# Kernel tuning notes

Hardware: AMD Instinct MI355X
Metric: run time of the kernel (lower is better)

The kernel has to match this reference:

```python
import jax, jax.numpy as jnp
import numpy as np

D = 256
H = 8
FFN = 2048
EPS = 1e-5


def _layer_norm(x, g, b):
    m = jnp.mean(x, axis=-1, keepdims=True)
    v = jnp.mean((x - m) ** 2, axis=-1, keepdims=True)
    return (x - m) * jax.lax.rsqrt(v + EPS) * g + b


def _mha(q_in, k_in, v_in, wq, bq, wk, bk, wv, bv, wo, bo, mask):
    B, Sq, _ = q_in.shape
    Sk = k_in.shape[1]
    dh = D // H
    q = (q_in @ wq + bq).reshape(B, Sq, H, dh)
    k = (k_in @ wk + bk).reshape(B, Sk, H, dh)
    v = (v_in @ wv + bv).reshape(B, Sk, H, dh)
    scores = jnp.einsum('bqhd,bkhd->bhqk', q, k) / jnp.sqrt(jnp.float32(dh)).astype(q.dtype)
    if mask is not None:
        scores = scores + mask
    probs = jax.nn.softmax(scores, axis=-1)
    ctx = jnp.einsum('bhqk,bkhd->bqhd', probs, v).reshape(B, Sq, D)
    return ctx @ wo + bo


def setup_inputs() -> dict:
    key = jax.random.key(0)
    ks = jax.random.split(key, 32)
    s = 0.02
    def lin(i, din, dout):
        return jax.random.normal(ks[i], (din, dout), jnp.float32) * s
    inp = {
        'vision_encoder_hidden_states': jax.random.normal(ks[0], (4, 2048, D), jnp.float32),
        'text_encoder_hidden_states': jax.random.normal(ks[1], (4, 1024, D), jnp.float32),
        'vision_encoder_attention_mask': jnp.zeros((4, 1, 1, 2048), jnp.float32),
        'text_encoder_attention_mask': jnp.zeros((4, 1, 1, 1024), jnp.float32),
        'sa_wq': lin(2, D, D), 'sa_bq': jnp.zeros((D,), jnp.float32),
        'sa_wk': lin(3, D, D), 'sa_bk': jnp.zeros((D,), jnp.float32),
        'sa_wv': lin(4, D, D), 'sa_bv': jnp.zeros((D,), jnp.float32),
        'sa_wo': lin(5, D, D), 'sa_bo': jnp.zeros((D,), jnp.float32),
        'ca_wq': lin(6, D, D), 'ca_bq': jnp.zeros((D,), jnp.float32),
        'ca_wk': lin(7, D, D), 'ca_bk': jnp.zeros((D,), jnp.float32),
        'ca_wv': lin(8, D, D), 'ca_bv': jnp.zeros((D,), jnp.float32),
        'ca_wo': lin(9, D, D), 'ca_bo': jnp.zeros((D,), jnp.float32),
        'ln1_g': jnp.ones((D,), jnp.float32), 'ln1_b': jnp.zeros((D,), jnp.float32),
        'ln2_g': jnp.ones((D,), jnp.float32), 'ln2_b': jnp.zeros((D,), jnp.float32),
        'ln3_g': jnp.ones((D,), jnp.float32), 'ln3_b': jnp.zeros((D,), jnp.float32),
        'ln4_g': jnp.ones((D,), jnp.float32), 'ln4_b': jnp.zeros((D,), jnp.float32),
        'fc1_w': lin(10, D, FFN), 'fc1_b': jnp.zeros((FFN,), jnp.float32),
        'fc2_w': lin(11, FFN, D), 'fc2_b': jnp.zeros((D,), jnp.float32),
    }
    return inp


def reference(vision_encoder_hidden_states, text_encoder_hidden_states,
              vision_encoder_attention_mask, text_encoder_attention_mask,
              sa_wq, sa_bq, sa_wk, sa_bk, sa_wv, sa_bv, sa_wo, sa_bo,
              ca_wq, ca_bq, ca_wk, ca_bk, ca_wv, ca_bv, ca_wo, ca_bo,
              ln1_g, ln1_b, ln2_g, ln2_b, ln3_g, ln3_b, ln4_g, ln4_b,
              fc1_w, fc1_b, fc2_w, fc2_b):
    # self-attention over vision queries (dropout = identity in eval)
    residual = vision_encoder_hidden_states
    h = _mha(vision_encoder_hidden_states, vision_encoder_hidden_states,
             vision_encoder_hidden_states,
             sa_wq, sa_bq, sa_wk, sa_bk, sa_wv, sa_bv, sa_wo, sa_bo,
             vision_encoder_attention_mask)
    h = _layer_norm(residual + h, ln1_g, ln1_b)
    # text cross-attention
    res2 = h
    h = _mha(h, text_encoder_hidden_states, text_encoder_hidden_states,
             ca_wq, ca_bq, ca_wk, ca_bk, ca_wv, ca_bv, ca_wo, ca_bo,
             text_encoder_attention_mask)
    h = _layer_norm(res2 + h, ln2_g, ln2_b)
    # third block: residual + dropout(h) -> in eval this is h + h = 2h, then LN
    h = _layer_norm(h + h, ln3_g, ln3_b)
    # FFN
    res = h
    h = jax.nn.relu(h @ fc1_w + fc1_b)
    h = h @ fc2_w + fc2_b
    h = _layer_norm(res + h, ln4_g, ln4_b)
    return h
```

## Files before the change

### kernel.cpp

```cpp
#include <hip/hip_runtime.h>
#include <stdint.h>
#include <stddef.h>

#define HEADS 8
#define DH 32
#define DMODEL 256
#define LN_EPS 1e-5f
#define LOG2E 1.4426950408889634f
#define QSCALE 0.17677669529663687f
#define QSCALE2 (QSCALE * LOG2E)
#define EXP2(x) __builtin_amdgcn_exp2f(x)

typedef unsigned short u16;
typedef __bf16 bf16x8 __attribute__((ext_vector_type(8)));
typedef unsigned short u16x8 __attribute__((ext_vector_type(8)));
typedef float f32x4 __attribute__((ext_vector_type(4)));

static __device__ __forceinline__ u16 bfc(float f) {
    return __builtin_bit_cast(u16, (__bf16)f);
}
static __device__ __forceinline__ bf16x8 ldbf8(const u16* p) {
    return __builtin_bit_cast(bf16x8, *reinterpret_cast<const u16x8*>(p));
}
static __device__ __forceinline__ bf16x8 cvt8(float4 a, float4 b) {
    bf16x8 r;
    r[0] = (__bf16)a.x; r[1] = (__bf16)a.y; r[2] = (__bf16)a.z; r[3] = (__bf16)a.w;
    r[4] = (__bf16)b.x; r[5] = (__bf16)b.y; r[6] = (__bf16)b.z; r[7] = (__bf16)b.w;
    return r;
}

struct TDesc { const float* src; u16* dst; int K; int N; };
struct TArgs { TDesc d[10]; };

__global__ __launch_bounds__(256) void transpose_cvt(TArgs args) {
    TDesc d = args.d[blockIdx.y];
    const int ntx = d.N >> 5;
    const int tiles = (d.K >> 5) * ntx;
    if ((int)blockIdx.x >= tiles) return;
    const int tk = (blockIdx.x / ntx) << 5;
    const int tn = (blockIdx.x % ntx) << 5;
    __shared__ float t[32][33];
    const int lx = threadIdx.x & 31;
    const int ly = threadIdx.x >> 5;
#pragma unroll
    for (int i = 0; i < 4; ++i)
        t[ly + 8 * i][lx] = d.src[(size_t)(tk + ly + 8 * i) * d.N + tn + lx];
    __syncthreads();
#pragma unroll
    for (int i = 0; i < 4; ++i)
        d.dst[(size_t)(tn + ly + 8 * i) * d.K + tk + lx] = bfc(t[lx][ly + 8 * i]);
}

struct Slice { u16* out; const float* bias; int mode; float sc; };

__global__ __launch_bounds__(256) void gemm_xproj(
    const float* __restrict__ Af, const u16* __restrict__ Wt,
    Slice s0, Slice s1, Slice s2, int M, int ntm)
{
    const int lane = threadIdx.x & 63;
    const int wave = threadIdx.x >> 6;
    const int l15 = lane & 15, lhi = lane >> 4;
    const int tm = ((int)blockIdx.x % ntm) * 128;
    const int tn = ((int)blockIdx.x / ntm) * 64;
    const int wm = tm + wave * 32;
    const int sel = tn >> 8;
    const int tl = tn & 255;
    Slice sl = (sel == 0) ? s0 : (sel == 1 ? s1 : s2);

    const f32x4 z4 = {0.f, 0.f, 0.f, 0.f};
    f32x4 acc[2][4];
#pragma unroll
    for (int i = 0; i < 2; ++i)
#pragma unroll
        for (int j = 0; j < 4; ++j) acc[i][j] = z4;

    const float* ar0 = Af + (size_t)(wm + l15) * 256 + lhi * 8;
    const float* ar1 = ar0 + (size_t)16 * 256;
    const u16* b0p = Wt + (size_t)(tn + l15) * 256 + lhi * 8;

    float4 a00 = *(const float4*)(ar0), a01 = *(const float4*)(ar0 + 4);
    float4 a10 = *(const float4*)(ar1), a11 = *(const float4*)(ar1 + 4);
    bf16x8 b[4];
#pragma unroll
    for (int j = 0; j < 4; ++j) b[j] = ldbf8(b0p + (size_t)j * 16 * 256);

#pragma unroll
    for (int k = 32; k < 256; k += 32) {
        float4 n00 = *(const float4*)(ar0 + k), n01 = *(const float4*)(ar0 + k + 4);
        float4 n10 = *(const float4*)(ar1 + k), n11 = *(const float4*)(ar1 + k + 4);
        bf16x8 bn[4];
#pragma unroll
        for (int j = 0; j < 4; ++j) bn[j] = ldbf8(b0p + (size_t)j * 16 * 256 + k);
        bf16x8 a0 = cvt8(a00, a01), a1 = cvt8(a10, a11);
#pragma unroll
        for (int j = 0; j < 4; ++j) {
            acc[0][j] = __builtin_amdgcn_mfma_f32_16x16x32_bf16(a0, b[j], acc[0][j], 0, 0, 0);
            acc[1][j] = __builtin_amdgcn_mfma_f32_16x16x32_bf16(a1, b[j], acc[1][j], 0, 0, 0);
        }
        a00 = n00; a01 = n01; a10 = n10; a11 = n11;
#pragma unroll
        for (int j = 0; j < 4; ++j) b[j] = bn[j];
    }
    {
        bf16x8 a0 = cvt8(a00, a01), a1 = cvt8(a10, a11);
#pragma unroll
        for (int j = 0; j < 4; ++j) {
            acc[0][j] = __builtin_amdgcn_mfma_f32_16x16x32_bf16(a0, b[j], acc[0][j], 0, 0, 0);
            acc[1][j] = __builtin_amdgcn_mfma_f32_16x16x32_bf16(a1, b[j], acc[1][j], 0, 0, 0);
        }
    }

#pragma unroll
    for (int i = 0; i < 2; ++i) {
#pragma unroll
        for (int j = 0; j < 4; ++j) {
            const int col = tl + j * 16 + l15;
            const float bv = sl.bias[col];
            const int row0 = wm + i * 16 + lhi * 4;
            if (sl.mode == 1) {
#pragma unroll
                for (int r = 0; r < 4; ++r)
                    sl.out[(size_t)(row0 + r) * 256 + col] = bfc((acc[i][j][r] + bv) * sl.sc);
            } else {
                ushort4 o = make_ushort4(bfc((acc[i][j][0] + bv) * sl.sc), bfc((acc[i][j][1] + bv) * sl.sc),
                                         bfc((acc[i][j][2] + bv) * sl.sc), bfc((acc[i][j][3] + bv) * sl.sc));
                *reinterpret_cast<ushort4*>(sl.out + (size_t)col * M + row0) = o;
            }
        }
    }
}

template<int MODE, bool RELU>
__global__ __launch_bounds__(256) void gemm_wide(
    const u16* __restrict__ A, const u16* __restrict__ Bt,
    const float* __restrict__ bias, void* __restrict__ Cout,
    int M, int N, int K, int ntm, float osc)
{
    const int lane = threadIdx.x & 63;
    const int wave = threadIdx.x >> 6;
    const int l15 = lane & 15, lhi = lane >> 4;
    const int tm = ((int)blockIdx.x % ntm) * 128;
    const int tn = ((int)blockIdx.x / ntm) * 128;
    const int wm = tm + wave * 32;

    const f32x4 z4 = {0.f, 0.f, 0.f, 0.f};
    f32x4 acc[2][8];
#pragma unroll
    for (int i = 0; i < 2; ++i)
#pragma unroll
        for (int j = 0; j < 8; ++j) acc[i][j] = z4;

    const u16* a0p = A + (size_t)(wm + l15) * K + lhi * 8;
    const u16* a1p = a0p + (size_t)16 * K;
    const u16* b0p = Bt + (size_t)(tn + l15) * K + lhi * 8;

    bf16x8 a0 = ldbf8(a0p), a1 = ldbf8(a1p);
    bf16x8 b[8];
#pragma unroll
    for (int j = 0; j < 8; ++j) b[j] = ldbf8(b0p + (size_t)j * 16 * K);

    for (int k = 32; k < K; k += 32) {
        bf16x8 a0n = ldbf8(a0p + k), a1n = ldbf8(a1p + k);
        bf16x8 bn[8];
#pragma unroll
        for (int j = 0; j < 8; ++j) bn[j] = ldbf8(b0p + (size_t)j * 16 * K + k);
#pragma unroll
        for (int j = 0; j < 8; ++j) {
            acc[0][j] = __builtin_amdgcn_mfma_f32_16x16x32_bf16(a0, b[j], acc[0][j], 0, 0, 0);
            acc[1][j] = __builtin_amdgcn_mfma_f32_16x16x32_bf16(a1, b[j], acc[1][j], 0, 0, 0);
        }
        a0 = a0n; a1 = a1n;
#pragma unroll
        for (int j = 0; j < 8; ++j) b[j] = bn[j];
    }
#pragma unroll
    for (int j = 0; j < 8; ++j) {
        acc[0][j] = __builtin_amdgcn_mfma_f32_16x16x32_bf16(a0, b[j], acc[0][j], 0, 0, 0);
        acc[1][j] = __builtin_amdgcn_mfma_f32_16x16x32_bf16(a1, b[j], acc[1][j], 0, 0, 0);
    }

#pragma unroll
    for (int i = 0; i < 2; ++i) {
#pragma unroll
        for (int j = 0; j < 8; ++j) {
            const int col = tn + j * 16 + l15;
            const float bv = bias[col];
            const int row0 = wm + i * 16 + lhi * 4;
            if (MODE == 0) {
                float* C = (float*)Cout;
#pragma unroll
                for (int r = 0; r < 4; ++r) {
                    float v = acc[i][j][r] + bv;
                    if (RELU) v = fmaxf(v, 0.f);
                    C[(size_t)(row0 + r) * N + col] = v;
                }
            } else {
                u16* C = (u16*)Cout;
#pragma unroll
                for (int r = 0; r < 4; ++r) {
                    float v = acc[i][j][r] + bv;
                    if (RELU) v = fmaxf(v, 0.f);
                    C[(size_t)(row0 + r) * N + col] = bfc(v * osc);
                }
            }
        }
    }
}

__global__ __launch_bounds__(256) void gemm_sk2(
    const u16* __restrict__ A, const u16* __restrict__ Bt,
    const float* __restrict__ bias, float* __restrict__ Cout,
    int M, int N, int lda, int Kh, int ntm)
{
    const int kh = (int)blockIdx.x >= (ntm * (N / 64));
    const int bid = (int)blockIdx.x - kh * (ntm * (N / 64));
    const int lane = threadIdx.x & 63;
    const int wave = threadIdx.x >> 6;
    const int l15 = lane & 15, lhi = lane >> 4;
    const int tm = (bid % ntm) * 128;
    const int tn = (bid / ntm) * 64;
    const int wm = tm + wave * 32;

    const f32x4 z4 = {0.f, 0.f, 0.f, 0.f};
    f32x4 acc[2][4];
#pragma unroll
    for (int i = 0; i < 2; ++i)
#pragma unroll
        for (int j = 0; j < 4; ++j) acc[i][j] = z4;

    const u16* a0p = A + (size_t)(wm + l15) * lda + kh * Kh + lhi * 8;
    const u16* a1p = a0p + (size_t)16 * lda;
    const u16* b0p = Bt + (size_t)(tn + l15) * lda + kh * Kh + lhi * 8;

    bf16x8 a0 = ldbf8(a0p), a1 = ldbf8(a1p);
    bf16x8 b[4];
#pragma unroll
    for (int j = 0; j < 4; ++j) b[j] = ldbf8(b0p + (size_t)j * 16 * lda);

    for (int k = 32; k < Kh; k += 32) {
        bf16x8 a0n = ldbf8(a0p + k), a1n = ldbf8(a1p + k);
        bf16x8 bn[4];
#pragma unroll
        for (int j = 0; j < 4; ++j) bn[j] = ldbf8(b0p + (size_t)j * 16 * lda + k);
#pragma unroll
        for (int j = 0; j < 4; ++j) {
            acc[0][j] = __builtin_amdgcn_mfma_f32_16x16x32_bf16(a0, b[j], acc[0][j], 0, 0, 0);
            acc[1][j] = __builtin_amdgcn_mfma_f32_16x16x32_bf16(a1, b[j], acc[1][j], 0, 0, 0);
        }
        a0 = a0n; a1 = a1n;
#pragma unroll
        for (int j = 0; j < 4; ++j) b[j] = bn[j];
    }
#pragma unroll
    for (int j = 0; j < 4; ++j) {
        acc[0][j] = __builtin_amdgcn_mfma_f32_16x16x32_bf16(a0, b[j], acc[0][j], 0, 0, 0);
        acc[1][j] = __builtin_amdgcn_mfma_f32_16x16x32_bf16(a1, b[j], acc[1][j], 0, 0, 0);
    }

    float* C = Cout + (size_t)kh * M * N;
    const float bs = kh ? 0.f : 1.f;
#pragma unroll
    for (int i = 0; i < 2; ++i) {
#pragma unroll
        for (int j = 0; j < 4; ++j) {
            const int col = tn + j * 16 + l15;
            const float bv = bias[col] * bs;
            const int row0 = wm + i * 16 + lhi * 4;
#pragma unroll
            for (int r = 0; r < 4; ++r)
                C[(size_t)(row0 + r) * N + col] = acc[i][j][r] + bv;
        }
    }
}

template<int MODE, bool RELU>
__global__ __launch_bounds__(256) void gemm64(
    const u16* __restrict__ A, const u16* __restrict__ Bt,
    const float* __restrict__ bias, void* __restrict__ Cout,
    int M, int N, int K, int ntn, float osc)
{
    const int lane = threadIdx.x & 63;
    const int wave = threadIdx.x >> 6;
    const int l15 = lane & 15, lhi = lane >> 4;
    const int tn = ((int)blockIdx.x % ntn) * 64;
    const int tm = ((int)blockIdx.x / ntn) * 64;
    const int wm = tm + (wave & 1) * 32;
    const int wn = tn + (wave >> 1) * 32;

    const f32x4 z4 = {0.f, 0.f, 0.f, 0.f};
    f32x4 acc[2][2] = {{z4, z4}, {z4, z4}};

    const u16* a0p = A + (size_t)(wm + l15) * K + lhi * 8;
    const u16* a1p = a0p + (size_t)16 * K;
    const u16* b0p = Bt + (size_t)(wn + l15) * K + lhi * 8;
    const u16* b1p = b0p + (size_t)16 * K;

    bf16x8 aA0 = ldbf8(a0p), aA1 = ldbf8(a1p), bA0 = ldbf8(b0p), bA1 = ldbf8(b1p);
    bf16x8 aB0 = ldbf8(a0p + 32), aB1 = ldbf8(a1p + 32), bB0 = ldbf8(b0p + 32), bB1 = ldbf8(b1p + 32);

#define G64_MFMA(aX0, aX1, bX0, bX1)                                                        \
    acc[0][0] = __builtin_amdgcn_mfma_f32_16x16x32_bf16(aX0, bX0, acc[0][0], 0, 0, 0);      \
    acc[0][1] = __builtin_amdgcn_mfma_f32_16x16x32_bf16(aX0, bX1, acc[0][1], 0, 0, 0);      \
    acc[1][0] = __builtin_amdgcn_mfma_f32_16x16x32_bf16(aX1, bX0, acc[1][0], 0, 0, 0);      \
    acc[1][1] = __builtin_amdgcn_mfma_f32_16x16x32_bf16(aX1, bX1, acc[1][1], 0, 0, 0);

    for (int k = 64; k < K; k += 64) {
        G64_MFMA(aA0, aA1, bA0, bA1);
        aA0 = ldbf8(a0p + k); aA1 = ldbf8(a1p + k);
        bA0 = ldbf8(b0p + k); bA1 = ldbf8(b1p + k);
        G64_MFMA(aB0, aB1, bB0, bB1);
        aB0 = ldbf8(a0p + k + 32); aB1 = ldbf8(a1p + k + 32);
        bB0 = ldbf8(b0p + k + 32); bB1 = ldbf8(b1p + k + 32);
    }
    G64_MFMA(aA0, aA1, bA0, bA1);
    G64_MFMA(aB0, aB1, bB0, bB1);
#undef G64_MFMA

#pragma unroll
    for (int i = 0; i < 2; ++i) {
#pragma unroll
        for (int j = 0; j < 2; ++j) {
            const int col = wn + j * 16 + l15;
            const float bv = bias[col];
            const int row0 = wm + i * 16 + lhi * 4;
            if (MODE == 0) {
                float* C = (float*)Cout;
#pragma unroll
                for (int r = 0; r < 4; ++r) {
                    float v = acc[i][j][r] + bv;
                    if (RELU) v = fmaxf(v, 0.f);
                    C[(size_t)(row0 + r) * N + col] = v;
                }
            } else {
                u16* C = (u16*)Cout;
#pragma unroll
                for (int r = 0; r < 4; ++r) {
                    float v = acc[i][j][r] + bv;
                    if (RELU) v = fmaxf(v, 0.f);
                    C[(size_t)(row0 + r) * N + col] = bfc(v * osc);
                }
            }
        }
    }
}

__global__ __launch_bounds__(256) void attn_kernel(
    const u16* __restrict__ Qb, const u16* __restrict__ Kb,
    const u16* __restrict__ Vt, const float* __restrict__ mask,
    u16* __restrict__ Ob, int Sq, int Sk, int MkTot)
{
    const int wave = threadIdx.x >> 6;
    const int lane = threadIdx.x & 63;
    const int l15 = lane & 15, lhi = lane >> 4;
    const int nqc = Sq >> 7;

    const int nwg = (int)gridDim.x;
    const int p = (int)blockIdx.x;
    const int wgid = (p & 7) * (nwg >> 3) + (p >> 3);

    const int bh = wgid / nqc;
    const int qc = wgid % nqc;
    const int b = bh >> 3;
    const int h = bh & 7;
    const int colh = h * DH;
    const int qrow0 = b * Sq + (qc << 7) + wave * 32;
    const int swz = (l15 & 8) << 1;

    __shared__ __align__(16) u16 pt[4][32][72];

    const f32x4 z4 = {0.f, 0.f, 0.f, 0.f};
    const bf16x8 qf0 = ldbf8(Qb + (size_t)(qrow0 + l15) * DMODEL + colh + lhi * 8);
    const bf16x8 qf1 = ldbf8(Qb + (size_t)(qrow0 + 16 + l15) * DMODEL + colh + lhi * 8);

    f32x4 ctx[2][2] = {{z4, z4}, {z4, z4}};
    float m0 = -1e30f, m1 = -1e30f, ss0 = 0.f, ss1 = 0.f;

    const float* mb = mask + (size_t)b * Sk;
    const u16* kbase = Kb + (size_t)(b * Sk) * DMODEL + colh + lhi * 8;
    const u16* vbase = Vt + (size_t)colh * MkTot + (size_t)b * Sk;

    bf16x8 kf[4], vf[4];
    float4 mk[4];
#pragma unroll
    for (int j = 0; j < 4; ++j)
        kf[j] = ldbf8(kbase + (size_t)(j * 16 + l15) * DMODEL);
#pragma unroll
    for (int ks = 0; ks < 2; ++ks)
#pragma unroll
        for (int dt = 0; dt < 2; ++dt)
            vf[ks * 2 + dt] = ldbf8(vbase + (size_t)(dt * 16 + l15) * MkTot + ks * 32 + lhi * 8);
#pragma unroll
    for (int j = 0; j < 4; ++j) {
        float4 t0 = *reinterpret_cast<const float4*>(mb + j * 16 + lhi * 4);
        mk[j] = make_float4(t0.x * LOG2E, t0.y * LOG2E, t0.z * LOG2E, t0.w * LOG2E);
    }

    for (int kt = 0; kt < Sk; kt += 64) {
        f32x4 s[2][4];
#pragma unroll
        for (int j = 0; j < 4; ++j) {
            s[0][j] = __builtin_amdgcn_mfma_f32_16x16x32_bf16(kf[j], qf0, z4, 0, 0, 0);
            s[1][j] = __builtin_amdgcn_mfma_f32_16x16x32_bf16(kf[j], qf1, z4, 0, 0, 0);
        }

        const int ktn = (kt + 64 < Sk) ? kt + 64 : kt;
        bf16x8 kn[4], vn[4];
        float4 mn[4];
#pragma unroll
        for (int j = 0; j < 4; ++j)
            kn[j] = ldbf8(kbase + (size_t)(ktn + j * 16 + l15) * DMODEL);
#pragma unroll
        for (int ks = 0; ks < 2; ++ks)
#pragma unroll
            for (int dt = 0; dt < 2; ++dt)
                vn[ks * 2 + dt] = ldbf8(vbase + (size_t)(dt * 16 + l15) * MkTot + ktn + ks * 32 + lhi * 8);
#pragma unroll
        for (int j = 0; j < 4; ++j)
            mn[j] = *reinterpret_cast<const float4*>(mb + ktn + j * 16 + lhi * 4);

#pragma unroll
        for (int j = 0; j < 4; ++j) {
            s[0][j][0] += mk[j].x; s[1][j][0] += mk[j].x;
            s[0][j][1] += mk[j].y; s[1][j][1] += mk[j].y;
            s[0][j][2] += mk[j].z; s[1][j][2] += mk[j].z;
            s[0][j][3] += mk[j].w; s[1][j][3] += mk[j].w;
        }

        float mx0 = fmaxf(fmaxf(s[0][0][0], s[0][0][1]), fmaxf(s[0][0][2], s[0][0][3]));
        float mx1 = fmaxf(fmaxf(s[1][0][0], s[1][0][1]), fmaxf(s[1][0][2], s[1][0][3]));
#pragma unroll
        for (int j = 1; j < 4; ++j) {
            mx0 = fmaxf(mx0, fmaxf(fmaxf(s[0][j][0], s[0][j][1]), fmaxf(s[0][j][2], s[0][j][3])));
            mx1 = fmaxf(mx1, fmaxf(fmaxf(s[1][j][0], s[1][j][1]), fmaxf(s[1][j][2], s[1][j][3])));
        }

        if (!__all((mx0 - m0 <= 12.0f) && (mx1 - m1 <= 12.0f))) {
            mx0 = fmaxf(mx0, __shfl_xor(mx0, 16, 64));
            mx0 = fmaxf(mx0, __shfl_xor(mx0, 32, 64));
            mx1 = fmaxf(mx1, __shfl_xor(mx1, 16, 64));
            mx1 = fmaxf(mx1, __shfl_xor(mx1, 32, 64));
            float n0 = fmaxf(m0, mx0), n1 = fmaxf(m1, mx1);
            float c0 = EXP2(m0 - n0), c1 = EXP2(m1 - n1);
            m0 = n0; m1 = n1; ss0 *= c0; ss1 *= c1;
#pragma unroll
            for (int r = 0; r < 4; ++r) {
                float cc0 = __shfl(c0, lhi * 4 + r, 64);
                float cc1 = __shfl(c1, lhi * 4 + r, 64);
                ctx[0][0][r] *= cc0; ctx[0][1][r] *= cc0;
                ctx[1][0][r] *= cc1; ctx[1][1][r] *= cc1;
            }
        }

        float pa0 = 0.f, pb0 = 0.f, pc0 = 0.f, pd0 = 0.f;
        float pa1 = 0.f, pb1 = 0.f, pc1 = 0.f, pd1 = 0.f;
#pragma unroll
        for (int j = 0; j < 4; ++j) {
            float e00 = EXP2(s[0][j][0] - m0), e01 = EXP2(s[0][j][1] - m0);
            float e02 = EXP2(s[0][j][2] - m0), e03 = EXP2(s[0][j][3] - m0);
            float e10 = EXP2(s[1][j][0] - m1), e11 = EXP2(s[1][j][1] - m1);
            float e12 = EXP2(s[1][j][2] - m1), e13 = EXP2(s[1][j][3] - m1);
            s[0][j][0] = e00; s[0][j][1] = e01; s[0][j][2] = e02; s[0][j][3] = e03;
            s[1][j][0] = e10; s[1][j][1] = e11; s[1][j][2] = e12; s[1][j][3] = e13;
            pa0 += e00; pb0 += e01; pc0 += e02; pd0 += e03;
            pa1 += e10; pb1 += e11; pc1 += e12; pd1 += e13;
        }
        ss0 += (pa0 + pb0) + (pc0 + pd0);
        ss1 += (pa1 + pb1) + (pc1 + pd1);

        asm volatile("" ::: "memory");
#pragma unroll
        for (int i = 0; i < 2; ++i)
#pragma unroll
            for (int j = 0; j < 4; ++j) {
                ushort4 w = make_ushort4(bfc(s[i][j][0]), bfc(s[i][j][1]),
                                         bfc(s[i][j][2]), bfc(s[i][j][3]));
                *reinterpret_cast<ushort4*>(&pt[wave][i * 16 + l15][(j * 16 + lhi * 4) ^ swz]) = w;
            }
        asm volatile("" ::: "memory");

#pragma unroll
        for (int ks = 0; ks < 2; ++ks) {
            bf16x8 pa = ldbf8(&pt[wave][l15][(ks * 32 + lhi * 8) ^ swz]);
            bf16x8 pb = ldbf8(&pt[wave][16 + l15][(ks * 32 + lhi * 8) ^ swz]);
#pragma unroll
            for (int dt = 0; dt < 2; ++dt) {
                ctx[0][dt] = __builtin_amdgcn_mfma_f32_16x16x32_bf16(pa, vf[ks * 2 + dt], ctx[0][dt], 0, 0, 0);
                ctx[1][dt] = __builtin_amdgcn_mfma_f32_16x16x32_bf16(pb, vf[ks * 2 + dt], ctx[1][dt], 0, 0, 0);
            }
        }

#pragma unroll
        for (int j = 0; j < 4; ++j) { kf[j] = kn[j]; vf[j] = vn[j]; mk[j] = mn[j]; }
    }

    ss0 += __shfl_xor(ss0, 16, 64); ss0 += __shfl_xor(ss0, 32, 64);
    ss1 += __shfl_xor(ss1, 16, 64); ss1 += __shfl_xor(ss1, 32, 64);
#pragma unroll
    for (int r = 0; r < 4; ++r) {
        const float i0 = 1.0f / __shfl(ss0, lhi * 4 + r, 64);
        const float i1 = 1.0f / __shfl(ss1, lhi * 4 + r, 64);
        const int row0 = qrow0 + lhi * 4 + r;
#pragma unroll
        for (int dt = 0; dt < 2; ++dt) {
            Ob[(size_t)row0 * DMODEL + colh + dt * 16 + l15] = bfc(ctx[0][dt][r] * i0);
            Ob[(size_t)(row0 + 16) * DMODEL + colh + dt * 16 + l15] = bfc(ctx[1][dt][r] * i1);
        }
    }
}

template<bool DBL, bool WBF, bool SPLIT>
__global__ __launch_bounds__(256) void ln_kernel(
    const float* __restrict__ X, const float* __restrict__ X2, const float* __restrict__ Res,
    const float* __restrict__ g1p, const float* __restrict__ b1p,
    const float* __restrict__ g2p, const float* __restrict__ b2p,
    float* __restrict__ Of, u16* __restrict__ Oh)
{
    const int lane = threadIdx.x & 63;
    const int row = blockIdx.x * 4 + (threadIdx.x >> 6);
    const size_t base = (size_t)row * DMODEL + lane * 4;
    float4 x = *reinterpret_cast<const float4*>(X + base);
    float4 rr = *reinterpret_cast<const float4*>(Res + base);
    float v[4] = {x.x + rr.x, x.y + rr.y, x.z + rr.z, x.w + rr.w};
    if constexpr (SPLIT) {
        float4 x2 = *reinterpret_cast<const float4*>(X2 + base);
        v[0] += x2.x; v[1] += x2.y; v[2] += x2.z; v[3] += x2.w;
    }
    float s = v[0] + v[1] + v[2] + v[3];
    float q = v[0] * v[0] + v[1] * v[1] + v[2] * v[2] + v[3] * v[3];
#pragma unroll
    for (int m = 1; m < 64; m <<= 1) { s += __shfl_xor(s, m, 64); q += __shfl_xor(q, m, 64); }
    float mean = s * (1.0f / DMODEL);
    float rstd = rsqrtf(fmaxf(q * (1.0f / DMODEL) - mean * mean, 0.f) + LN_EPS);
    float4 g = *reinterpret_cast<const float4*>(g1p + lane * 4);
    float4 bb = *reinterpret_cast<const float4*>(b1p + lane * 4);
    float y[4];
    y[0] = (v[0] - mean) * rstd * g.x + bb.x;
    y[1] = (v[1] - mean) * rstd * g.y + bb.y;
    y[2] = (v[2] - mean) * rstd * g.z + bb.z;
    y[3] = (v[3] - mean) * rstd * g.w + bb.w;
    if constexpr (DBL) {
#pragma unroll
        for (int k2 = 0; k2 < 4; ++k2) y[k2] *= 2.0f;
        float s2 = y[0] + y[1] + y[2] + y[3];
        float q2 = y[0] * y[0] + y[1] * y[1] + y[2] * y[2] + y[3] * y[3];
#pragma unroll
        for (int m = 1; m < 64; m <<= 1) { s2 += __shfl_xor(s2, m, 64); q2 += __shfl_xor(q2, m, 64); }
        float mean2 = s2 * (1.0f / DMODEL);
        float rstd2 = rsqrtf(fmaxf(q2 * (1.0f / DMODEL) - mean2 * mean2, 0.f) + LN_EPS);
        float4 g2 = *reinterpret_cast<const float4*>(g2p + lane * 4);
        float4 b2 = *reinterpret_cast<const float4*>(b2p + lane * 4);
        y[0] = (y[0] - mean2) * rstd2 * g2.x + b2.x;
        y[1] = (y[1] - mean2) * rstd2 * g2.y + b2.y;
        y[2] = (y[2] - mean2) * rstd2 * g2.z + b2.z;
        y[3] = (y[3] - mean2) * rstd2 * g2.w + b2.w;
    }
    *reinterpret_cast<float4*>(Of + base) = make_float4(y[0], y[1], y[2], y[3]);
    if constexpr (WBF) {
        ushort4 o = make_ushort4(bfc(y[0]), bfc(y[1]), bfc(y[2]), bfc(y[3]));
        *reinterpret_cast<ushort4*>(Oh + base) = o;
    }
}

extern "C" void kernel_launch(void* const* d_in, const int* in_sizes, int n_in,
                              void* d_out, int out_size, void* d_ws, size_t ws_size,
                              hipStream_t stream) {
    constexpr size_t MB = 1u << 20;
    if (ws_size < 70 * MB) return;

    const float* vis   = (const float*)d_in[0];
    const float* txt   = (const float*)d_in[1];
    const float* vmask = (const float*)d_in[2];
    const float* tmask = (const float*)d_in[3];
    const float* sa_wq = (const float*)d_in[4];  const float* sa_bq = (const float*)d_in[5];
    const float* sa_wk = (const float*)d_in[6];  const float* sa_bk = (const float*)d_in[7];
    const float* sa_wv = (const float*)d_in[8];  const float* sa_bv = (const float*)d_in[9];
    const float* sa_wo = (const float*)d_in[10]; const float* sa_bo = (const float*)d_in[11];
    const float* ca_wq = (const float*)d_in[12]; const float* ca_bq = (const float*)d_in[13];
    const float* ca_wk = (const float*)d_in[14]; const float* ca_bk = (const float*)d_in[15];
    const float* ca_wv = (const float*)d_in[16]; const float* ca_bv = (const float*)d_in[17];
    const float* ca_wo = (const float*)d_in[18]; const float* ca_bo = (const float*)d_in[19];
    const float* ln1_g = (const float*)d_in[20]; const float* ln1_b = (const float*)d_in[21];
    const float* ln2_g = (const float*)d_in[22]; const float* ln2_b = (const float*)d_in[23];
    const float* ln3_g = (const float*)d_in[24]; const float* ln3_b = (const float*)d_in[25];
    const float* ln4_g = (const float*)d_in[26]; const float* ln4_b = (const float*)d_in[27];
    const float* fc1_w = (const float*)d_in[28]; const float* fc1_b = (const float*)d_in[29];
    const float* fc2_w = (const float*)d_in[30]; const float* fc2_b = (const float*)d_in[31];

    const int B = 4, Sq = 2048, St = 1024;
    const int Mq = B * Sq;
    const int Mt = B * St;

    char* ws = (char*)d_ws;
    u16*   q_bf    = (u16*)(ws + 6 * MB);
    u16*   k_bf    = (u16*)(ws + 10 * MB);
    u16*   vt_bf   = (u16*)(ws + 14 * MB);
    u16*   ctx_bf  = (u16*)(ws + 18 * MB);
    u16*   ffn1_bf = (u16*)(ws + 0);
    float* attn_f  = (float*)(ws + 32 * MB);
    float* h1_f    = (float*)(ws + 40 * MB);
    u16*   h1_bf   = (u16*)(ws + 48 * MB);
    float* h3_f    = (float*)(ws + 52 * MB);
    u16*   h3_bf   = (u16*)(ws + 60 * MB);
    u16*   wts     = (u16*)(ws + 64 * MB);
    float* ffn2a   = attn_f;
    float* ffn2b   = h1_f;

    u16* wqkv_t = wts;
    u16* wkv_t  = wqkv_t + 768 * 256;
    u16* cwq_t  = wkv_t + 512 * 256;
    u16* wo_t   = cwq_t + 65536;
    u16* cwo_t  = wo_t + 65536;
    u16* fc1_t  = cwo_t + 65536;
    u16* fc2_t  = fc1_t + 2048 * 256;

    TArgs ta;
    ta.d[0] = {sa_wq, wqkv_t + 0 * 65536, 256, 256};
    ta.d[1] = {sa_wk, wqkv_t + 1 * 65536, 256, 256};
    ta.d[2] = {sa_wv, wqkv_t + 2 * 65536, 256, 256};
    ta.d[3] = {ca_wk, wkv_t + 0 * 65536, 256, 256};
    ta.d[4] = {ca_wv, wkv_t + 1 * 65536, 256, 256};
    ta.d[5] = {ca_wq, cwq_t, 256, 256};
    ta.d[6] = {sa_wo, wo_t, 256, 256};
    ta.d[7] = {ca_wo, cwo_t, 256, 256};
    ta.d[8] = {fc1_w, fc1_t, 256, 2048};
    ta.d[9] = {fc2_w, fc2_t, 2048, 256};
    transpose_cvt<<<dim3(512, 10), 256, 0, stream>>>(ta);

    Slice sq = {q_bf, sa_bq, 1, QSCALE2}, sk = {k_bf, sa_bk, 1, 1.f}, sv = {vt_bf, sa_bv, 2, 1.f};
    gemm_xproj<<<dim3((Mq / 128) * 12), 256, 0, stream>>>(vis, wqkv_t, sq, sk, sv, Mq, Mq / 128);
    attn_kernel<<<dim3(B * HEADS * (Sq / 128)), 256, 0, stream>>>(q_bf, k_bf, vt_bf, vmask, ctx_bf, Sq, Sq, Mq);
    gemm64<0, false><<<dim3((Mq / 64) * 4), 256, 0, stream>>>(ctx_bf, wo_t, sa_bo, attn_f, Mq, 256, 256, 4, 1.f);
    ln_kernel<false, true, false><<<dim3(Mq / 4), 256, 0, stream>>>(attn_f, nullptr, vis, ln1_g, ln1_b, nullptr, nullptr, h1_f, h1_bf);

    Slice ck = {k_bf, ca_bk, 1, 1.f}, cv = {vt_bf, ca_bv, 2, 1.f}, cd = {nullptr, nullptr, 1, 1.f};
    gemm_xproj<<<dim3((Mt / 128) * 8), 256, 0, stream>>>(txt, wkv_t, ck, cv, cd, Mt, Mt / 128);
    gemm64<1, false><<<dim3((Mq / 64) * 4), 256, 0, stream>>>(h1_bf, cwq_t, ca_bq, q_bf, Mq, 256, 256, 4, QSCALE2);
    attn_kernel<<<dim3(B * HEADS * (Sq / 128)), 256, 0, stream>>>(q_bf, k_bf, vt_bf, tmask, ctx_bf, Sq, St, Mt);
    gemm64<0, false><<<dim3((Mq / 64) * 4), 256, 0, stream>>>(ctx_bf, cwo_t, ca_bo, attn_f, Mq, 256, 256, 4, 1.f);
    ln_kernel<true, true, false><<<dim3(Mq / 4), 256, 0, stream>>>(attn_f, nullptr, h1_f, ln2_g, ln2_b, ln3_g, ln3_b, h3_f, h3_bf);

    gemm_wide<1, true><<<dim3((Mq / 128) * 16), 256, 0, stream>>>(h3_bf, fc1_t, fc1_b, ffn1_bf, Mq, 2048, 256, Mq / 128, 1.f);
    gemm_sk2<<<dim3((Mq / 128) * 4 * 2), 256, 0, stream>>>(ffn1_bf, fc2_t, fc2_b, ffn2a, Mq, 256, 2048, 1024, Mq / 128);
    ln_kernel<false, false, true><<<dim3(Mq / 4), 256, 0, stream>>>(ffn2a, ffn2b, h3_f, ln4_g, ln4_b, nullptr, nullptr, (float*)d_out, nullptr);
}
```

Before: 290.1 us.

## Process 64 query rows per wave in attention, drop K/V register prefetch

Each attention wave now handles four 16-row query groups instead of two, so a workgroup covers 256 query rows and half as many workgroups launch. Each K/V/mask tile loaded from global memory is reused across twice as many query rows, cutting redundant K/V traffic. The software prefetch of the next K/V tile into registers is removed and loads now happen at the top of each iteration, which exposes load latency. Register pressure also rises from the larger score and context arrays. The grid halves to 256 blocks, which may underfill a 256-CU device.

```diff
diff --git a/kernel.cpp b/kernel.cpp
--- a/kernel.cpp
+++ b/kernel.cpp
@@ -352,7 +352,7 @@
     const int wave = threadIdx.x >> 6;
     const int lane = threadIdx.x & 63;
     const int l15 = lane & 15, lhi = lane >> 4;
-    const int nqc = Sq >> 7;
+    const int nqc = Sq >> 8;
 
     const int nwg = (int)gridDim.x;
     const int p = (int)blockIdx.x;
@@ -363,147 +363,140 @@
     const int b = bh >> 3;
     const int h = bh & 7;
     const int colh = h * DH;
-    const int qrow0 = b * Sq + (qc << 7) + wave * 32;
+    const int qrow0 = b * Sq + (qc << 8) + wave * 64;
     const int swz = (l15 & 8) << 1;
 
-    __shared__ __align__(16) u16 pt[4][32][72];
+    __shared__ __align__(16) u16 pt[4][64][72];
 
     const f32x4 z4 = {0.f, 0.f, 0.f, 0.f};
-    const bf16x8 qf0 = ldbf8(Qb + (size_t)(qrow0 + l15) * DMODEL + colh + lhi * 8);
-    const bf16x8 qf1 = ldbf8(Qb + (size_t)(qrow0 + 16 + l15) * DMODEL + colh + lhi * 8);
-
-    f32x4 ctx[2][2] = {{z4, z4}, {z4, z4}};
-    float m0 = -1e30f, m1 = -1e30f, ss0 = 0.f, ss1 = 0.f;
+    bf16x8 qf[4];
+#pragma unroll
+    for (int g = 0; g < 4; ++g)
+        qf[g] = ldbf8(Qb + (size_t)(qrow0 + g * 16 + l15) * DMODEL + colh + lhi * 8);
+
+    f32x4 ctx[4][2];
+#pragma unroll
+    for (int g = 0; g < 4; ++g) { ctx[g][0] = z4; ctx[g][1] = z4; }
+    float m[4] = {-1e30f, -1e30f, -1e30f, -1e30f};
+    float ss[4] = {0.f, 0.f, 0.f, 0.f};
 
     const float* mb = mask + (size_t)b * Sk;
     const u16* kbase = Kb + (size_t)(b * Sk) * DMODEL + colh + lhi * 8;
     const u16* vbase = Vt + (size_t)colh * MkTot + (size_t)b * Sk;
 
-    bf16x8 kf[4], vf[4];
-    float4 mk[4];
-#pragma unroll
-    for (int j = 0; j < 4; ++j)
-        kf[j] = ldbf8(kbase + (size_t)(j * 16 + l15) * DMODEL);
-#pragma unroll
-    for (int ks = 0; ks < 2; ++ks)
-#pragma unroll
-        for (int dt = 0; dt < 2; ++dt)
-            vf[ks * 2 + dt] = ldbf8(vbase + (size_t)(dt * 16 + l15) * MkTot + ks * 32 + lhi * 8);
-#pragma unroll
-    for (int j = 0; j < 4; ++j) {
-        float4 t0 = *reinterpret_cast<const float4*>(mb + j * 16 + lhi * 4);
-        mk[j] = make_float4(t0.x * LOG2E, t0.y * LOG2E, t0.z * LOG2E, t0.w * LOG2E);
-    }
-
     for (int kt = 0; kt < Sk; kt += 64) {
-        f32x4 s[2][4];
+        bf16x8 kf[4], vf[4];
+        float4 mk[4];
+#pragma unroll
+        for (int j = 0; j < 4; ++j)
+            kf[j] = ldbf8(kbase + (size_t)(kt + j * 16 + l15) * DMODEL);
+#pragma unroll
+        for (int ks = 0; ks < 2; ++ks)
+#pragma unroll
+            for (int dt = 0; dt < 2; ++dt)
+                vf[ks * 2 + dt] = ldbf8(vbase + (size_t)(dt * 16 + l15) * MkTot + kt + ks * 32 + lhi * 8);
 #pragma unroll
         for (int j = 0; j < 4; ++j) {
-            s[0][j] = __builtin_amdgcn_mfma_f32_16x16x32_bf16(kf[j], qf0, z4, 0, 0, 0);
-            s[1][j] = __builtin_amdgcn_mfma_f32_16x16x32_bf16(kf[j], qf1, z4, 0, 0, 0);
-        }
-
-        const int ktn = (kt + 64 < Sk) ? kt + 64 : kt;
-        bf16x8 kn[4], vn[4];
-        float4 mn[4];
-#pragma unroll
-        for (int j = 0; j < 4; ++j)
-            kn[j] = ldbf8(kbase + (size_t)(ktn + j * 16 + l15) * DMODEL);
-#pragma unroll
-        for (int ks = 0; ks < 2; ++ks)
-#pragma unroll
-            for (int dt = 0; dt < 2; ++dt)
-                vn[ks * 2 + dt] = ldbf8(vbase + (size_t)(dt * 16 + l15) * MkTot + ktn + ks * 32 + lhi * 8);
-#pragma unroll
-        for (int j = 0; j < 4; ++j)
-            mn[j] = *reinterpret_cast<const float4*>(mb + ktn + j * 16 + lhi * 4);
-
-#pragma unroll
-        for (int j = 0; j < 4; ++j) {
-            s[0][j][0] += mk[j].x; s[1][j][0] += mk[j].x;
-            s[0][j][1] += mk[j].y; s[1][j][1] += mk[j].y;
-            s[0][j][2] += mk[j].z; s[1][j][2] += mk[j].z;
-            s[0][j][3] += mk[j].w; s[1][j][3] += mk[j].w;
-        }
-
-        float mx0 = fmaxf(fmaxf(s[0][0][0], s[0][0][1]), fmaxf(s[0][0][2], s[0][0][3]));
-        float mx1 = fmaxf(fmaxf(s[1][0][0], s[1][0][1]), fmaxf(s[1][0][2], s[1][0][3]));
-#pragma unroll
-        for (int j = 1; j < 4; ++j) {
-            mx0 = fmaxf(mx0, fmaxf(fmaxf(s[0][j][0], s[0][j][1]), fmaxf(s[0][j][2], s[0][j][3])));
-            mx1 = fmaxf(mx1, fmaxf(fmaxf(s[1][j][0], s[1][j][1]), fmaxf(s[1][j][2], s[1][j][3])));
-        }
-
-        if (!__all((mx0 - m0 <= 12.0f) && (mx1 - m1 <= 12.0f))) {
-            mx0 = fmaxf(mx0, __shfl_xor(mx0, 16, 64));
-            mx0 = fmaxf(mx0, __shfl_xor(mx0, 32, 64));
-            mx1 = fmaxf(mx1, __shfl_xor(mx1, 16, 64));
-            mx1 = fmaxf(mx1, __shfl_xor(mx1, 32, 64));
-            float n0 = fmaxf(m0, mx0), n1 = fmaxf(m1, mx1);
-            float c0 = EXP2(m0 - n0), c1 = EXP2(m1 - n1);
-            m0 = n0; m1 = n1; ss0 *= c0; ss1 *= c1;
-#pragma unroll
-            for (int r = 0; r < 4; ++r) {
-                float cc0 = __shfl(c0, lhi * 4 + r, 64);
-                float cc1 = __shfl(c1, lhi * 4 + r, 64);
-                ctx[0][0][r] *= cc0; ctx[0][1][r] *= cc0;
-                ctx[1][0][r] *= cc1; ctx[1][1][r] *= cc1;
+            float4 t0 = *reinterpret_cast<const float4*>(mb + kt + j * 16 + lhi * 4);
+            mk[j] = make_float4(t0.x * LOG2E, t0.y * LOG2E, t0.z * LOG2E, t0.w * LOG2E);
+        }
+
+        f32x4 s[4][4];
+#pragma unroll
+        for (int g = 0; g < 4; ++g)
+#pragma unroll
+            for (int j = 0; j < 4; ++j)
+                s[g][j] = __builtin_amdgcn_mfma_f32_16x16x32_bf16(kf[j], qf[g], z4, 0, 0, 0);
+
+#pragma unroll
+        for (int g = 0; g < 4; ++g)
+#pragma unroll
+            for (int j = 0; j < 4; ++j) {
+                s[g][j][0] += mk[j].x; s[g][j][1] += mk[j].y;
+                s[g][j][2] += mk[j].z; s[g][j][3] += mk[j].w;
             }
-        }
-
-        float pa0 = 0.f, pb0 = 0.f, pc0 = 0.f, pd0 = 0.f;
-        float pa1 = 0.f, pb1 = 0.f, pc1 = 0.f, pd1 = 0.f;
-#pragma unroll
-        for (int j = 0; j < 4; ++j) {
-            float e00 = EXP2(s[0][j][0] - m0), e01 = EXP2(s[0][j][1] - m0);
-            float e02 = EXP2(s[0][j][2] - m0), e03 = EXP2(s[0][j][3] - m0);
-            float e10 = EXP2(s[1][j][0] - m1), e11 = EXP2(s[1][j][1] - m1);
-            float e12 = EXP2(s[1][j][2] - m1), e13 = EXP2(s[1][j][3] - m1);
-            s[0][j][0] = e00; s[0][j][1] = e01; s[0][j][2] = e02; s[0][j][3] = e03;
-            s[1][j][0] = e10; s[1][j][1] = e11; s[1][j][2] = e12; s[1][j][3] = e13;
-            pa0 += e00; pb0 += e01; pc0 += e02; pd0 += e03;
-            pa1 += e10; pb1 += e11; pc1 += e12; pd1 += e13;
-        }
-        ss0 += (pa0 + pb0) + (pc0 + pd0);
-        ss1 += (pa1 + pb1) + (pc1 + pd1);
+
+        float mx[4];
+#pragma unroll
+        for (int g = 0; g < 4; ++g) {
+            float v0 = fmaxf(fmaxf(s[g][0][0], s[g][0][1]), fmaxf(s[g][0][2], s[g][0][3]));
+            float v1 = fmaxf(fmaxf(s[g][1][0], s[g][1][1]), fmaxf(s[g][1][2], s[g][1][3]));
+            float v2 = fmaxf(fmaxf(s[g][2][0], s[g][2][1]), fmaxf(s[g][2][2], s[g][2][3]));
+            float v3 = fmaxf(fmaxf(s[g][3][0], s[g][3][1]), fmaxf(s[g][3][2], s[g][3][3]));
+            mx[g] = fmaxf(fmaxf(v0, v1), fmaxf(v2, v3));
+        }
+
+        bool ok = (mx[0] - m[0] <= 12.0f) && (mx[1] - m[1] <= 12.0f) &&
+                  (mx[2] - m[2] <= 12.0f) && (mx[3] - m[3] <= 12.0f);
+        if (!__all(ok)) {
+#pragma unroll
+            for (int g = 0; g < 4; ++g) {
+                float v = mx[g];
+                v = fmaxf(v, __shfl_xor(v, 16, 64));
+                v = fmaxf(v, __shfl_xor(v, 32, 64));
+                float n = fmaxf(m[g], v);
+                float c = EXP2(m[g] - n);
+                m[g] = n; ss[g] *= c;
+#pragma unroll
+                for (int r = 0; r < 4; ++r) {
+                    float cc = __shfl(c, lhi * 4 + r, 64);
+                    ctx[g][0][r] *= cc; ctx[g][1][r] *= cc;
+                }
+            }
+        }
+
+#pragma unroll
+        for (int g = 0; g < 4; ++g) {
+            float pa = 0.f, pb = 0.f, pc = 0.f, pd = 0.f;
+#pragma unroll
+            for (int j = 0; j < 4; ++j) {
+                float e0 = EXP2(s[g][j][0] - m[g]);
+                float e1 = EXP2(s[g][j][1] - m[g]);
+                float e2 = EXP2(s[g][j][2] - m[g]);
+                float e3 = EXP2(s[g][j][3] - m[g]);
+                s[g][j][0] = e0; s[g][j][1] = e1; s[g][j][2] = e2; s[g][j][3] = e3;
+                pa += e0; pb += e1; pc += e2; pd += e3;
+            }
+            ss[g] += (pa + pb) + (pc + pd);
+        }
 
         asm volatile("" ::: "memory");
 #pragma unroll
-        for (int i = 0; i < 2; ++i)
+        for (int g = 0; g < 4; ++g)
 #pragma unroll
             for (int j = 0; j < 4; ++j) {
-                ushort4 w = make_ushort4(bfc(s[i][j][0]), bfc(s[i][j][1]),
-                                         bfc(s[i][j][2]), bfc(s[i][j][3]));
-                *reinterpret_cast<ushort4*>(&pt[wave][i * 16 + l15][(j * 16 + lhi * 4) ^ swz]) = w;
+                ushort4 w = make_ushort4(bfc(s[g][j][0]), bfc(s[g][j][1]),
+                                         bfc(s[g][j][2]), bfc(s[g][j][3]));
+                *reinterpret_cast<ushort4*>(&pt[wave][g * 16 + l15][(j * 16 + lhi * 4) ^ swz]) = w;
             }
         asm volatile("" ::: "memory");
 
 #pragma unroll
         for (int ks = 0; ks < 2; ++ks) {
-            bf16x8 pa = ldbf8(&pt[wave][l15][(ks * 32 + lhi * 8) ^ swz]);
-            bf16x8 pb = ldbf8(&pt[wave][16 + l15][(ks * 32 + lhi * 8) ^ swz]);
-#pragma unroll
-            for (int dt = 0; dt < 2; ++dt) {
-                ctx[0][dt] = __builtin_amdgcn_mfma_f32_16x16x32_bf16(pa, vf[ks * 2 + dt], ctx[0][dt], 0, 0, 0);
-                ctx[1][dt] = __builtin_amdgcn_mfma_f32_16x16x32_bf16(pb, vf[ks * 2 + dt], ctx[1][dt], 0, 0, 0);
-            }
-        }
-
-#pragma unroll
-        for (int j = 0; j < 4; ++j) { kf[j] = kn[j]; vf[j] = vn[j]; mk[j] = mn[j]; }
-    }
-
-    ss0 += __shfl_xor(ss0, 16, 64); ss0 += __shfl_xor(ss0, 32, 64);
-    ss1 += __shfl_xor(ss1, 16, 64); ss1 += __shfl_xor(ss1, 32, 64);
-#pragma unroll
-    for (int r = 0; r < 4; ++r) {
-        const float i0 = 1.0f / __shfl(ss0, lhi * 4 + r, 64);
-        const float i1 = 1.0f / __shfl(ss1, lhi * 4 + r, 64);
-        const int row0 = qrow0 + lhi * 4 + r;
-#pragma unroll
-        for (int dt = 0; dt < 2; ++dt) {
-            Ob[(size_t)row0 * DMODEL + colh + dt * 16 + l15] = bfc(ctx[0][dt][r] * i0);
-            Ob[(size_t)(row0 + 16) * DMODEL + colh + dt * 16 + l15] = bfc(ctx[1][dt][r] * i1);
+            bf16x8 pa[4];
+#pragma unroll
+            for (int g = 0; g < 4; ++g)
+                pa[g] = ldbf8(&pt[wave][g * 16 + l15][(ks * 32 + lhi * 8) ^ swz]);
+#pragma unroll
+            for (int g = 0; g < 4; ++g)
+#pragma unroll
+                for (int dt = 0; dt < 2; ++dt)
+                    ctx[g][dt] = __builtin_amdgcn_mfma_f32_16x16x32_bf16(pa[g], vf[ks * 2 + dt], ctx[g][dt], 0, 0, 0);
+        }
+    }
+
+#pragma unroll
+    for (int g = 0; g < 4; ++g) {
+        float v = ss[g];
+        v += __shfl_xor(v, 16, 64);
+        v += __shfl_xor(v, 32, 64);
+#pragma unroll
+        for (int r = 0; r < 4; ++r) {
+            const float inv = 1.0f / __shfl(v, lhi * 4 + r, 64);
+            const int row = qrow0 + g * 16 + lhi * 4 + r;
+#pragma unroll
+            for (int dt = 0; dt < 2; ++dt)
+                Ob[(size_t)row * DMODEL + colh + dt * 16 + l15] = bfc(ctx[g][dt][r] * inv);
         }
     }
 }
@@ -628,14 +621,14 @@
 
     Slice sq = {q_bf, sa_bq, 1, QSCALE2}, sk = {k_bf, sa_bk, 1, 1.f}, sv = {vt_bf, sa_bv, 2, 1.f};
     gemm_xproj<<<dim3((Mq / 128) * 12), 256, 0, stream>>>(vis, wqkv_t, sq, sk, sv, Mq, Mq / 128);
-    attn_kernel<<<dim3(B * HEADS * (Sq / 128)), 256, 0, stream>>>(q_bf, k_bf, vt_bf, vmask, ctx_bf, Sq, Sq, Mq);
+    attn_kernel<<<dim3(B * HEADS * (Sq / 256)), 256, 0, stream>>>(q_bf, k_bf, vt_bf, vmask, ctx_bf, Sq, Sq, Mq);
     gemm64<0, false><<<dim3((Mq / 64) * 4), 256, 0, stream>>>(ctx_bf, wo_t, sa_bo, attn_f, Mq, 256, 256, 4, 1.f);
     ln_kernel<false, true, false><<<dim3(Mq / 4), 256, 0, stream>>>(attn_f, nullptr, vis, ln1_g, ln1_b, nullptr, nullptr, h1_f, h1_bf);
 
     Slice ck = {k_bf, ca_bk, 1, 1.f}, cv = {vt_bf, ca_bv, 2, 1.f}, cd = {nullptr, nullptr, 1, 1.f};
     gemm_xproj<<<dim3((Mt / 128) * 8), 256, 0, stream>>>(txt, wkv_t, ck, cv, cd, Mt, Mt / 128);
     gemm64<1, false><<<dim3((Mq / 64) * 4), 256, 0, stream>>>(h1_bf, cwq_t, ca_bq, q_bf, Mq, 256, 256, 4, QSCALE2);
-    attn_kernel<<<dim3(B * HEADS * (Sq / 128)), 256, 0, stream>>>(q_bf, k_bf, vt_bf, tmask, ctx_bf, Sq, St, Mt);
+    attn_kernel<<<dim3(B * HEADS * (Sq / 256)), 256, 0, stream>>>(q_bf, k_bf, vt_bf, tmask, ctx_bf, Sq, St, Mt);
     gemm64<0, false><<<dim3((Mq / 64) * 4), 256, 0, stream>>>(ctx_bf, cwo_t, ca_bo, attn_f, Mq, 256, 256, 4, 1.f);
     ln_kernel<true, true, false><<<dim3(Mq / 4), 256, 0, stream>>>(attn_f, nullptr, h1_f, ln2_g, ln2_b, ln3_g, ln3_b, h3_f, h3_bf);
 
```

Measured after the change: 283.0 us. 1.03x faster.
